# Optimization experiments

Hardware: AMD Instinct MI355X
Metric: run time of the kernel (lower is better)

## Reference

```python
import jax, jax.numpy as jnp
import numpy as np

B, NQ, L, E, K = 64, 1024, 128, 8192, 2
LN_EPS = 1e-5


def setup_inputs() -> dict:
    key = jax.random.key(0)
    ks = jax.random.split(key, 16)
    s1 = 1.0 / np.sqrt(2 * L + 1)
    s2 = 1.0 / np.sqrt(L)
    s3 = 1.0 / np.sqrt(2 * L)
    return {
        "z0": jax.random.normal(ks[0], (B, L), jnp.float32),
        "edge_index": jax.random.randint(ks[1], (2, E), 0, NQ, jnp.int64),
        "edge_attr": jax.random.normal(ks[2], (E,), jnp.float32),
        "n_qubits": NQ,
        # edge MLP params, stacked over K message-passing rounds
        "e_w1": jax.random.normal(ks[3], (K, L, 2 * L + 1), jnp.float32) * s1,
        "e_b1": jnp.zeros((K, L), jnp.float32),
        "e_w2": jax.random.normal(ks[4], (K, L, L), jnp.float32) * s2,
        "e_b2": jnp.zeros((K, L), jnp.float32),
        # node MLP params
        "n_w1": jax.random.normal(ks[5], (K, L, 2 * L), jnp.float32) * s3,
        "n_b1": jnp.zeros((K, L), jnp.float32),
        "ln_g": jnp.ones((K, L), jnp.float32),
        "ln_b": jnp.zeros((K, L), jnp.float32),
        "n_w2": jax.random.normal(ks[6], (K, L, L), jnp.float32) * s2,
        "n_b2": jnp.zeros((K, L), jnp.float32),
    }


def reference(z0, edge_index, edge_attr, n_qubits,
              e_w1, e_b1, e_w2, e_b2,
              n_w1, n_b1, ln_g, ln_b, n_w2, n_b2):
    b, l = z0.shape
    src, tgt = edge_index[0], edge_index[1]
    e_ = src.shape[0]
    # broadcast latent z0 to every node: h [B, N, L]
    h = jnp.broadcast_to(z0[:, None, :], (b, n_qubits, l))
    e = jnp.broadcast_to(edge_attr[None, :, None], (b, e_, 1))  # [B, E, 1]
    k_rounds = e_w1.shape[0]
    for k in range(k_rounds):
        hi = h[:, src, :]  # gather source node feats [B, E, L]
        hj = h[:, tgt, :]  # gather target node feats [B, E, L]
        inp_e = jnp.concatenate([hi, hj, e], axis=-1)  # [B, E, 2L+1]
        m = jax.nn.relu(inp_e @ e_w1[k].T + e_b1[k]) @ e_w2[k].T + e_b2[k]
        # scatter_add messages back to source nodes
        m_agg = jnp.zeros_like(h).at[:, src, :].add(m)
        inp_n = jnp.concatenate([h, m_agg], axis=-1)  # [B, N, 2L]
        x = jax.nn.relu(inp_n @ n_w1[k].T + n_b1[k])
        mu = x.mean(axis=-1, keepdims=True)
        var = ((x - mu) ** 2).mean(axis=-1, keepdims=True)
        x = (x - mu) * jax.lax.rsqrt(var + LN_EPS) * ln_g[k] + ln_b[k]
        # Dropout(p=0.1) is identity in eval mode
        h = x @ n_w2[k].T + n_b2[k] + h  # residual
    return h.mean(axis=1)  # [B, L]
```

## Files before the change

### kernel.cpp

```cpp
#include <hip/hip_runtime.h>

#define B_   64
#define NQ_  1024
#define L_   128
#define E_   8192
#define M_   (B_*NQ_)
#define LDP  136
#define TILE 2176

typedef unsigned short u16;
typedef unsigned int   u32;
typedef __attribute__((ext_vector_type(8))) short short8;
typedef __attribute__((ext_vector_type(4))) float floatx4;

#define WVB() __builtin_amdgcn_wave_barrier()

__device__ __forceinline__ u16 f2bf(float f) {
    union { float f; u32 u; } v; v.f = f;
    return (u16)((v.u + 0x7fffu + ((v.u >> 16) & 1u)) >> 16);
}
__device__ __forceinline__ float bf2f(u16 u) {
    union { u32 u; float f; } v; v.u = ((u32)u) << 16;
    return v.f;
}
__device__ __forceinline__ floatx4 mfma16(short8 a, short8 b, floatx4 c) {
    return __builtin_amdgcn_mfma_f32_16x16x32_bf16(a, b, c, 0, 0, 0);
}
__device__ __forceinline__ short8 gfrag(const u16* base, int r0, int kb, int lane) {
    return *(const short8*)(base + (size_t)(r0 + (lane & 15)) * 128 + kb * 32 + (lane >> 4) * 8);
}
__device__ __forceinline__ short8 sfrag(const u16* t, int r0, int kb, int lane) {
    return *(const short8*)(t + (r0 + (lane & 15)) * LDP + kb * 32 + (lane >> 4) * 8);
}
__device__ __forceinline__ short8 wfrag(const u16* wf, int nt, int kb, int lane) {
    return *(const short8*)(wf + (((kb << 3) + nt) * 64 + lane) * 8);
}
__device__ __forceinline__ void frag_flush(const u16* t, u16* wf, int nt, int lane) {
#pragma unroll
    for (int kb = 0; kb < 4; ++kb)
        *(short8*)(wf + (((kb << 3) + nt) * 64 + lane) * 8) = sfrag(t, 0, kb, lane);
}
__device__ __forceinline__ short8 frag_cvt(const float* base, int r0, int ld, int kb, int lane) {
    const float* p = base + (size_t)(r0 + (lane & 15)) * ld + kb * 32 + (lane >> 4) * 8;
    short8 s;
#pragma unroll
    for (int j = 0; j < 8; ++j) s[j] = (short)f2bf(p[j]);
    return s;
}
__device__ __forceinline__ void tile_store(u16* t, const floatx4* acc, int lane) {
    int col = lane & 15, qd = lane >> 4;
#pragma unroll
    for (int nt = 0; nt < 8; ++nt)
#pragma unroll
        for (int r = 0; r < 4; ++r)
            t[(qd * 4 + r) * LDP + nt * 16 + col] = f2bf(acc[nt][r]);
}
__device__ __forceinline__ void tile_flush(const u16* t, u16* g, int lane) {
#pragma unroll
    for (int it = 0; it < 4; ++it) {
        int chunk = it * 64 + lane, row = chunk >> 4, c8 = chunk & 15;
        *(uint4*)(g + (size_t)row * 128 + c8 * 8) = *(const uint4*)(t + row * LDP + c8 * 8);
    }
}

struct P {
    const int* ei; const float* attr; const float* z0;
    const float* e_w1; const float* e_b1; const float* e_w2; const float* e_b2;
    const float* n_w1; const float* n_b1; const float* ln_g; const float* ln_b;
    const float* n_w2; const float* n_b2;
    int* ofs; int* tgt_s; float* a_s; float* degf;
    u16* wf;
    u16* w_n20;
    float* wl; float* vb2;
    float* rx; float* rci; float* rcj; float* rh; float* mx0;
    u16* c0t; u16* S; u16* t1g; u16* ci1; u16* cj1;
    float* out;
};

__global__ __launch_bounds__(256) void k_setup(P p) {
    __shared__ __align__(16) char smem[52224];
    int tid = threadIdx.x, blk = blockIdx.x;
    int lane = tid & 63, w = tid >> 6, col = lane & 15, qd = lane >> 4;

    if (blk == 0) {
        int* cnt  = (int*)smem;
        int* wsum = cnt + 1024;
        int* flag = wsum + 8;
#pragma unroll
        for (int i = 0; i < 4; ++i) cnt[tid + i * 256] = 0;
        if (tid == 0) *flag = 1;
        __syncthreads();
        if (tid < 100 && p.ei[2 * tid + 1] != 0) atomicAnd(flag, 0);
        __syncthreads();
        int i64 = *flag;
        for (int e = tid; e < E_; e += 256) {
            int s = i64 ? p.ei[2 * e] : p.ei[e];
            atomicAdd(&cnt[s], 1);
        }
        __syncthreads();
        int q0 = tid * 4;
        int c0 = cnt[q0], c1 = cnt[q0 + 1], c2 = cnt[q0 + 2], c3 = cnt[q0 + 3];
        int tsum = c0 + c1 + c2 + c3, incl = tsum;
#pragma unroll
        for (int o = 1; o < 64; o <<= 1) {
            int t = __shfl_up(incl, o, 64);
            if (lane >= o) incl += t;
        }
        if (lane == 63) wsum[w] = incl;
        __syncthreads();
        int wo = 0;
        for (int i = 0; i < w; ++i) wo += wsum[i];
        int base = wo + incl - tsum;
        p.ofs[q0] = base; p.ofs[q0 + 1] = base + c0;
        p.ofs[q0 + 2] = base + c0 + c1; p.ofs[q0 + 3] = base + c0 + c1 + c2;
        p.degf[q0] = (float)c0; p.degf[q0 + 1] = (float)c1;
        p.degf[q0 + 2] = (float)c2; p.degf[q0 + 3] = (float)c3;
        if (tid == 0) p.ofs[NQ_] = E_;
        __syncthreads();
        cnt[q0] = base; cnt[q0 + 1] = base + c0;
        cnt[q0 + 2] = base + c0 + c1; cnt[q0 + 3] = base + c0 + c1 + c2;
        __syncthreads();
        for (int e = tid; e < E_; e += 256) {
            int s = i64 ? p.ei[2 * e]        : p.ei[e];
            int t = i64 ? p.ei[2 * (E_ + e)] : p.ei[E_ + e];
            int pos = atomicAdd(&cnt[s], 1);
            p.tgt_s[pos] = t;
            p.a_s[pos]   = p.attr[e];
        }
    } else if (blk == 1) {
        for (int idx = tid; idx < 16384; idx += 256) p.w_n20[idx] = f2bf(p.n_w2[idx]);
    } else if (blk == 2) {
        const float* src = p.n_w2 + 16384;
        u16* dst = p.wf + 5 * 16384;
        for (int pr = w; pr < 32; pr += 4) {
            int kb = pr >> 3, nt = pr & 7;
            const float* s = src + (nt * 16 + (lane & 15)) * 128 + kb * 32 + (lane >> 4) * 8;
            short8 v;
#pragma unroll
            for (int j = 0; j < 8; ++j) v[j] = (short)f2bf(s[j]);
            *(short8*)(dst + (pr * 64 + lane) * 8) = v;
        }
    } else if (blk <= 7) {
        const float* Pm; const float* Q; int ldp; u16* D;
        switch (blk) {
            case 3: Pm = p.n_w1 + 128;             ldp = 256; Q = p.e_w2;         D = p.wf;             break;
            case 4: Pm = p.n_w1 + 32768 + 128;     ldp = 256; Q = p.e_w2 + 16384; D = p.wf + 4 * 16384; break;
            case 5: Pm = p.e_w1 + 128 * 257;       ldp = 257; Q = p.n_w2;         D = p.wf + 1 * 16384; break;
            case 6: Pm = p.e_w1 + 128 * 257 + 128; ldp = 257; Q = p.n_w2;         D = p.wf + 2 * 16384; break;
            default:Pm = p.n_w1 + 32768;           ldp = 256; Q = p.n_w2;         D = p.wf + 3 * 16384; break;
        }
        u16* qt = (u16*)smem;
        u16* tl = (u16*)(smem + 34816);
        for (int idx = tid; idx < 16384; idx += 256) {
            int c = idx >> 7, kd = idx & 127;
            qt[kd * LDP + c] = f2bf(Q[idx]);
        }
        __syncthreads();
        for (int t = 0; t < 2; ++t) {
            int r0 = (w * 2 + t) * 16;
            floatx4 acc[8] = {};
#pragma unroll
            for (int kb = 0; kb < 4; ++kb) {
                short8 a = frag_cvt(Pm, r0, ldp, kb, lane);
#pragma unroll
                for (int nt = 0; nt < 8; ++nt)
                    acc[nt] = mfma16(a, sfrag(qt, nt * 16, kb, lane), acc[nt]);
            }
            u16* slot = tl + w * TILE;
            tile_store(slot, acc, lane); WVB();
            frag_flush(slot, D, w * 2 + t, lane); WVB();
        }
    } else if (blk == 8) {
        int r0 = w * 16;
        floatx4 acc[8] = {};
#pragma unroll
        for (int kb = 0; kb < 4; ++kb) {
            short8 a = frag_cvt(p.z0, r0, 128, kb, lane);
#pragma unroll
            for (int nt = 0; nt < 8; ++nt)
                acc[nt] = mfma16(a, frag_cvt(p.n_w1, nt * 16, 256, kb, lane), acc[nt]);
        }
#pragma unroll
        for (int nt = 0; nt < 8; ++nt) {
            int cg = nt * 16 + col; float bv = p.n_b1[cg];
#pragma unroll
            for (int r = 0; r < 4; ++r) p.rx[(r0 + qd * 4 + r) * 128 + cg] = acc[nt][r] + bv;
        }
    } else if (blk <= 11) {
        int r0 = w * 16;
        const float* Wp; int ld; const float* bias; float* dst;
        if (blk == 9)       { Wp = p.e_w1 + 128 * 257;       ld = 257; bias = p.e_b1 + 128; dst = p.rci; }
        else if (blk == 10) { Wp = p.e_w1 + 128 * 257 + 128; ld = 257; bias = nullptr;      dst = p.rcj; }
        else                { Wp = p.n_w1 + 32768;           ld = 256; bias = p.n_b1 + 128; dst = p.rh;  }
        floatx4 acc[8] = {};
#pragma unroll
        for (int kb = 0; kb < 4; ++kb) {
            short8 a;
            int rr = (r0 + (lane & 15)) * 128, kk = kb * 32 + (lane >> 4) * 8;
#pragma unroll
            for (int j = 0; j < 8; ++j) a[j] = (short)f2bf(p.z0[rr + kk + j] + p.n_b2[kk + j]);
#pragma unroll
            for (int nt = 0; nt < 8; ++nt)
                acc[nt] = mfma16(a, frag_cvt(Wp, nt * 16, ld, kb, lane), acc[nt]);
        }
#pragma unroll
        for (int nt = 0; nt < 8; ++nt) {
            int cg = nt * 16 + col;
            float bv = bias ? bias[cg] : 0.0f;
#pragma unroll
            for (int r = 0; r < 4; ++r) dst[(r0 + qd * 4 + r) * 128 + cg] = acc[nt][r] + bv;
        }
    } else if (blk == 12) {
        u16* tl = (u16*)(smem + 34816);
        int r0 = w * 16;
        floatx4 a1[8] = {};
#pragma unroll
        for (int kb = 0; kb < 4; ++kb) {
            short8 a = frag_cvt(p.z0, r0, 128, kb, lane);
#pragma unroll
            for (int nt = 0; nt < 8; ++nt) {
                a1[nt] = mfma16(a, frag_cvt(p.e_w1,       nt * 16, 257, kb, lane), a1[nt]);
                a1[nt] = mfma16(a, frag_cvt(p.e_w1 + 128, nt * 16, 257, kb, lane), a1[nt]);
            }
        }
#pragma unroll
        for (int nt = 0; nt < 8; ++nt) {
            float bv = p.e_b1[nt * 16 + col];
#pragma unroll
            for (int r = 0; r < 4; ++r) a1[nt][r] += bv;
        }
        u16* slot = tl + w * TILE;
        tile_store(slot, a1, lane); WVB();
        tile_flush(slot, p.c0t + (size_t)r0 * 128, lane);
    } else if (blk == 13) {
        int k = tid >> 7, c = tid & 127;
        float s = 0.0f;
        for (int n = 0; n < 128; ++n)
            s += p.n_w1[k * 32768 + c * 256 + 128 + n] * p.e_b2[k * 128 + n];
        p.vb2[tid] = s;
        p.wl[tid]  = p.e_w1[k * 128 * 257 + c * 257 + 256];
        for (int i = tid; i < 8192; i += 256) p.mx0[i] = 0.0f;
    }
}

__global__ __launch_bounds__(256) void k_edge(P p, int r0) {
    int tid = threadIdx.x, lane = tid & 63, w = tid >> 6;
    const u16* ci = r0 ? p.c0t : p.ci1;
    const u16* cj = p.cj1;
    const float* wl = r0 ? p.wl : p.wl + 128;
    float2 wl2 = ((const float2*)wl)[lane];
    int gw = blockIdx.x * 4 + w;
    int q = gw & (NQ_ - 1), bg = gw >> 10;
    int bl[8];
#pragma unroll
    for (int i = 0; i < 4; ++i) { bl[i] = bg * 4 + i; bl[i + 4] = bg * 4 + i + 32; }
    int st = p.ofs[q], en = p.ofs[q + 1];
    float ax[8] = {}, ay[8] = {};
    if (r0) {
        float cx[8], cy[8];
#pragma unroll
        for (int i = 0; i < 8; ++i) {
            u32 cv = ((const u32*)ci)[(size_t)bl[i] * 64 + lane];
            cx[i] = bf2f((u16)(cv & 0xffff)); cy[i] = bf2f((u16)(cv >> 16));
        }
        for (int idx = st; idx < en; ++idx) {
            float a = p.a_s[idx];
            float wx = a * wl2.x, wy = a * wl2.y;
#pragma unroll
            for (int i = 0; i < 8; ++i) {
                ax[i] += fmaxf(cx[i] + wx, 0.f);
                ay[i] += fmaxf(cy[i] + wy, 0.f);
            }
        }
    } else {
        const u32* cjp[8];
        float cx[8], cy[8];
#pragma unroll
        for (int i = 0; i < 8; ++i) {
            cjp[i] = (const u32*)cj + (size_t)bl[i] * NQ_ * 64;
            u32 cv = ((const u32*)ci)[((size_t)bl[i] * NQ_ + q) * 64 + lane];
            cx[i] = bf2f((u16)(cv & 0xffff)); cy[i] = bf2f((u16)(cv >> 16));
        }
        for (int idx = st; idx < en; ++idx) {
            int t = p.tgt_s[idx];
            float a = p.a_s[idx];
            size_t ro = (size_t)t * 64 + lane;
            float wx = a * wl2.x, wy = a * wl2.y;
#pragma unroll
            for (int i = 0; i < 8; ++i) {
                u32 jv = cjp[i][ro];
                ax[i] += fmaxf(cx[i] + bf2f((u16)(jv & 0xffff)) + wx, 0.f);
                ay[i] += fmaxf(cy[i] + bf2f((u16)(jv >> 16))    + wy, 0.f);
            }
        }
    }
    u32* Sp = (u32*)p.S;
#pragma unroll
    for (int i = 0; i < 8; ++i)
        Sp[((size_t)bl[i] * NQ_ + q) * 64 + lane] =
            (u32)f2bf(ax[i]) | ((u32)f2bf(ay[i]) << 16);
}

__global__ __launch_bounds__(256, 2) void k_node0(P p) {
    __shared__ __align__(16) char smem[52224];
    u16* xt = (u16*)smem;
    u16* ob = (u16*)(smem + 34816);
    int tid = threadIdx.x, lane = tid & 63, w = tid >> 6;
    int col = lane & 15, qd = lane >> 4;
    int blk = blockIdx.x;
    int rowbase = blk * 128 + w * 32;
    int b = blk >> 3;

    floatx4 xa[2][8] = {};
#pragma unroll
    for (int kb = 0; kb < 4; ++kb) {
        short8 Bv[8];
#pragma unroll
        for (int nt = 0; nt < 8; ++nt) Bv[nt] = wfrag(p.wf, nt, kb, lane);
#pragma unroll
        for (int t = 0; t < 2; ++t) {
            short8 a = gfrag(p.S, rowbase + t * 16, kb, lane);
#pragma unroll
            for (int nt = 0; nt < 8; ++nt) xa[t][nt] = mfma16(a, Bv[nt], xa[t][nt]);
        }
    }
    float s8[8] = {};
#pragma unroll
    for (int t = 0; t < 2; ++t) {
#pragma unroll
        for (int nt = 0; nt < 8; ++nt) {
            int cg = nt * 16 + col;
            float base = p.rx[b * 128 + cg], vb = p.vb2[cg];
#pragma unroll
            for (int r = 0; r < 4; ++r) {
                int row = rowbase + t * 16 + qd * 4 + r;
                xa[t][nt][r] = fmaxf(xa[t][nt][r] + base + p.degf[row & (NQ_ - 1)] * vb, 0.f);
            }
        }
#pragma unroll
        for (int r = 0; r < 4; ++r) {
            float s = 0.f, s2 = 0.f;
#pragma unroll
            for (int nt = 0; nt < 8; ++nt) { float v = xa[t][nt][r]; s += v; s2 += v * v; }
#pragma unroll
            for (int o = 1; o < 16; o <<= 1) { s += __shfl_xor(s, o, 64); s2 += __shfl_xor(s2, o, 64); }
            float mu = s * (1.f / 128.f), var = s2 * (1.f / 128.f) - mu * mu;
            float rs = rsqrtf(var + 1e-5f);
#pragma unroll
            for (int nt = 0; nt < 8; ++nt) {
                int cg = nt * 16 + col;
                float xv = (xa[t][nt][r] - mu) * rs * p.ln_g[cg] + p.ln_b[cg];
                xa[t][nt][r] = xv;
                s8[nt] += xv;
            }
        }
        tile_store(xt + (w * 2 + t) * TILE, xa[t], lane);
    }
#pragma unroll
    for (int nt = 0; nt < 8; ++nt) {
        s8[nt] += __shfl_xor(s8[nt], 16, 64);
        s8[nt] += __shfl_xor(s8[nt], 32, 64);
    }
    if (lane < 16) {
#pragma unroll
        for (int nt = 0; nt < 8; ++nt)
            atomicAdd(p.mx0 + b * 128 + nt * 16 + lane, s8[nt]);
    }
    WVB();
#pragma unroll
    for (int ph = 0; ph < 3; ++ph) {
        const u16* wfp = p.wf + ((ph == 0) ? 1 : (ph == 1) ? 2 : 3) * 16384;
        const float* rt = (ph == 0) ? p.rci : (ph == 1) ? p.rcj : p.rh;
        floatx4 ca[2][8] = {};
#pragma unroll
        for (int kb = 0; kb < 4; ++kb) {
            short8 Bv[8];
#pragma unroll
            for (int nt = 0; nt < 8; ++nt) Bv[nt] = wfrag(wfp, nt, kb, lane);
#pragma unroll
            for (int t = 0; t < 2; ++t) {
                short8 a = sfrag(xt + (w * 2 + t) * TILE, 0, kb, lane);
#pragma unroll
                for (int nt = 0; nt < 8; ++nt) ca[t][nt] = mfma16(a, Bv[nt], ca[t][nt]);
            }
        }
#pragma unroll
        for (int t = 0; t < 2; ++t)
#pragma unroll
            for (int nt = 0; nt < 8; ++nt) {
                float rc = rt[b * 128 + nt * 16 + col];
#pragma unroll
                for (int r = 0; r < 4; ++r) ca[t][nt][r] += rc;
            }
        u16* dst = (ph == 0) ? p.ci1 : (ph == 1) ? p.cj1 : p.t1g;
#pragma unroll
        for (int t = 0; t < 2; ++t) {
            tile_store(ob + w * TILE, ca[t], lane);
            WVB();
            tile_flush(ob + w * TILE, dst + (size_t)(rowbase + t * 16) * 128, lane);
            WVB();
        }
    }
}

__global__ __launch_bounds__(256, 2) void k_node1(P p) {
    __shared__ __align__(16) char smem[52224];
    u16* ob = (u16*)(smem + 34816);
    int tid = threadIdx.x, lane = tid & 63, w = tid >> 6;
    int col = lane & 15, qd = lane >> 4;
    int blk = blockIdx.x;
    int rowbase = blk * 128 + w * 32;
    int b = blk >> 3;

    const u16* wc1 = p.wf + 4 * 16384;
    floatx4 xa[2][8] = {};
#pragma unroll
    for (int kb = 0; kb < 4; ++kb) {
        short8 Bv[8];
#pragma unroll
        for (int nt = 0; nt < 8; ++nt) Bv[nt] = wfrag(wc1, nt, kb, lane);
#pragma unroll
        for (int t = 0; t < 2; ++t) {
            short8 a = gfrag(p.S, rowbase + t * 16, kb, lane);
#pragma unroll
            for (int nt = 0; nt < 8; ++nt) xa[t][nt] = mfma16(a, Bv[nt], xa[t][nt]);
        }
    }
    const float* vb21 = p.vb2 + 128;
#pragma unroll
    for (int t = 0; t < 2; ++t) {
#pragma unroll
        for (int nt = 0; nt < 8; ++nt) {
            int cg = nt * 16 + col;
            float vb = vb21[cg];
#pragma unroll
            for (int r = 0; r < 4; ++r) {
                int row = rowbase + t * 16 + qd * 4 + r;
                float tv = bf2f(p.t1g[(size_t)row * 128 + cg]);
                xa[t][nt][r] = fmaxf(xa[t][nt][r] + tv + p.degf[row & (NQ_ - 1)] * vb, 0.f);
            }
        }
#pragma unroll
        for (int r = 0; r < 4; ++r) {
            float s = 0.f, s2 = 0.f;
#pragma unroll
            for (int nt = 0; nt < 8; ++nt) { float v = xa[t][nt][r]; s += v; s2 += v * v; }
#pragma unroll
            for (int o = 1; o < 16; o <<= 1) { s += __shfl_xor(s, o, 64); s2 += __shfl_xor(s2, o, 64); }
            float mu = s * (1.f / 128.f), var = s2 * (1.f / 128.f) - mu * mu;
            float rs = rsqrtf(var + 1e-5f);
#pragma unroll
            for (int nt = 0; nt < 8; ++nt) {
                int cg = nt * 16 + col;
                xa[t][nt][r] = (xa[t][nt][r] - mu) * rs * p.ln_g[128 + cg] + p.ln_b[128 + cg];
            }
        }
    }
    const u16* n21 = p.wf + 5 * 16384;
    float s8[8] = {};
#pragma unroll
    for (int t = 0; t < 2; ++t) {
        WVB();
        tile_store(ob + w * TILE, xa[t], lane);
        WVB();
        floatx4 ma[8] = {};
#pragma unroll
        for (int kb = 0; kb < 4; ++kb) {
            short8 Bv[8];
#pragma unroll
            for (int nt = 0; nt < 8; ++nt) Bv[nt] = wfrag(n21, nt, kb, lane);
            short8 a = sfrag(ob + w * TILE, 0, kb, lane);
#pragma unroll
            for (int nt = 0; nt < 8; ++nt) ma[nt] = mfma16(a, Bv[nt], ma[nt]);
        }
#pragma unroll
        for (int nt = 0; nt < 8; ++nt)
#pragma unroll
            for (int r = 0; r < 4; ++r) s8[nt] += ma[nt][r];
    }
#pragma unroll
    for (int nt = 0; nt < 8; ++nt) {
        s8[nt] += __shfl_xor(s8[nt], 16, 64);
        s8[nt] += __shfl_xor(s8[nt], 32, 64);
    }
    if (lane < 16) {
#pragma unroll
        for (int nt = 0; nt < 8; ++nt)
            atomicAdd(p.out + b * 128 + nt * 16 + lane, s8[nt] * (1.f / 1024.f));
    }
    if ((blk & 7) == 0 && tid < 128) {
        int c = tid;
        const float* mx = p.mx0 + b * 128;
        float s = 0.f;
#pragma unroll 4
        for (int k = 0; k < 128; ++k) s += mx[k] * bf2f(p.w_n20[c * 128 + k]);
        float acc = p.z0[b * 128 + c] + p.n_b2[c] + p.n_b2[128 + c] + s * (1.f / 1024.f);
        atomicAdd(p.out + b * 128 + c, acc);
    }
}

extern "C" void kernel_launch(void* const* d_in, const int* in_sizes, int n_in,
                              void* d_out, int out_size, void* d_ws, size_t ws_size,
                              hipStream_t stream) {
    P p;
    p.z0   = (const float*)d_in[0];
    p.ei   = (const int*)d_in[1];
    p.attr = (const float*)d_in[2];
    p.e_w1 = (const float*)d_in[4];
    p.e_b1 = (const float*)d_in[5];
    p.e_w2 = (const float*)d_in[6];
    p.e_b2 = (const float*)d_in[7];
    p.n_w1 = (const float*)d_in[8];
    p.n_b1 = (const float*)d_in[9];
    p.ln_g = (const float*)d_in[10];
    p.ln_b = (const float*)d_in[11];
    p.n_w2 = (const float*)d_in[12];
    p.n_b2 = (const float*)d_in[13];
    p.out  = (float*)d_out;

    const size_t H = (size_t)M_ * L_;
    float* f  = (float*)d_ws;
    p.degf = f;
    p.a_s  = f + 1024;
    p.wl   = p.a_s + 8192;
    p.vb2  = p.wl + 256;
    p.rx   = p.vb2 + 256;
    p.rci  = p.rx + 8192;
    p.rcj  = p.rci + 8192;
    p.rh   = p.rcj + 8192;
    p.mx0  = p.rh + 8192;
    p.ofs  = (int*)(p.mx0 + 8192);
    p.tgt_s = p.ofs + 1056;
    p.wf    = (u16*)(p.tgt_s + 8192);
    p.w_n20 = p.wf + 6 * 16384;
    p.c0t   = p.w_n20 + 16384;
    p.S     = p.c0t + 8192;
    p.t1g   = p.S + H;
    p.ci1   = p.t1g + H;
    p.cj1   = p.ci1 + H;

    hipMemsetAsync(p.out, 0, 8192 * sizeof(float), stream);

    k_setup<<<14, 256, 0, stream>>>(p);
    k_edge<<<2048, 256, 0, stream>>>(p, 1);
    k_node0<<<512, 256, 0, stream>>>(p);
    k_edge<<<2048, 256, 0, stream>>>(p, 0);
    k_node1<<<512, 256, 0, stream>>>(p);
}
```

Baseline: 192.4 us.

## Fuse round-0 edge aggregation into node0 kernel, computing A fragments in registers

The round-0 edge message sum depends only on the per-batch latent and the edge attribute, so node0 now computes the aggregated S values directly into MFMA A-fragments in registers. This replaces a separate k_edge launch and the write and read of the S buffer through global memory. The edge kernel is specialised to the round-1 path only. In exchange each lane recomputes per-edge ReLU sums for its rows, which adds ALU work and register pressure inside node0.

```diff
diff --git a/kernel.cpp b/kernel.cpp
--- a/kernel.cpp
+++ b/kernel.cpp
@@ -243,11 +243,9 @@
     }
 }
 
-__global__ __launch_bounds__(256) void k_edge(P p, int r0) {
+__global__ __launch_bounds__(256) void k_edge(P p) {
     int tid = threadIdx.x, lane = tid & 63, w = tid >> 6;
-    const u16* ci = r0 ? p.c0t : p.ci1;
-    const u16* cj = p.cj1;
-    const float* wl = r0 ? p.wl : p.wl + 128;
+    const float* wl = p.wl + 128;
     float2 wl2 = ((const float2*)wl)[lane];
     int gw = blockIdx.x * 4 + w;
     int q = gw & (NQ_ - 1), bg = gw >> 10;
@@ -256,42 +254,24 @@
     for (int i = 0; i < 4; ++i) { bl[i] = bg * 4 + i; bl[i + 4] = bg * 4 + i + 32; }
     int st = p.ofs[q], en = p.ofs[q + 1];
     float ax[8] = {}, ay[8] = {};
-    if (r0) {
-        float cx[8], cy[8];
+    const u32* cjp[8];
+    float cx[8], cy[8];
+#pragma unroll
+    for (int i = 0; i < 8; ++i) {
+        cjp[i] = (const u32*)p.cj1 + (size_t)bl[i] * NQ_ * 64;
+        u32 cv = ((const u32*)p.ci1)[((size_t)bl[i] * NQ_ + q) * 64 + lane];
+        cx[i] = bf2f((u16)(cv & 0xffff)); cy[i] = bf2f((u16)(cv >> 16));
+    }
+    for (int idx = st; idx < en; ++idx) {
+        int t = p.tgt_s[idx];
+        float a = p.a_s[idx];
+        size_t ro = (size_t)t * 64 + lane;
+        float wx = a * wl2.x, wy = a * wl2.y;
 #pragma unroll
         for (int i = 0; i < 8; ++i) {
-            u32 cv = ((const u32*)ci)[(size_t)bl[i] * 64 + lane];
-            cx[i] = bf2f((u16)(cv & 0xffff)); cy[i] = bf2f((u16)(cv >> 16));
-        }
-        for (int idx = st; idx < en; ++idx) {
-            float a = p.a_s[idx];
-            float wx = a * wl2.x, wy = a * wl2.y;
-#pragma unroll
-            for (int i = 0; i < 8; ++i) {
-                ax[i] += fmaxf(cx[i] + wx, 0.f);
-                ay[i] += fmaxf(cy[i] + wy, 0.f);
-            }
-        }
-    } else {
-        const u32* cjp[8];
-        float cx[8], cy[8];
-#pragma unroll
-        for (int i = 0; i < 8; ++i) {
-            cjp[i] = (const u32*)cj + (size_t)bl[i] * NQ_ * 64;
-            u32 cv = ((const u32*)ci)[((size_t)bl[i] * NQ_ + q) * 64 + lane];
-            cx[i] = bf2f((u16)(cv & 0xffff)); cy[i] = bf2f((u16)(cv >> 16));
-        }
-        for (int idx = st; idx < en; ++idx) {
-            int t = p.tgt_s[idx];
-            float a = p.a_s[idx];
-            size_t ro = (size_t)t * 64 + lane;
-            float wx = a * wl2.x, wy = a * wl2.y;
-#pragma unroll
-            for (int i = 0; i < 8; ++i) {
-                u32 jv = cjp[i][ro];
-                ax[i] += fmaxf(cx[i] + bf2f((u16)(jv & 0xffff)) + wx, 0.f);
-                ay[i] += fmaxf(cy[i] + bf2f((u16)(jv >> 16))    + wy, 0.f);
-            }
+            u32 jv = cjp[i][ro];
+            ax[i] += fmaxf(cx[i] + bf2f((u16)(jv & 0xffff)) + wx, 0.f);
+            ay[i] += fmaxf(cy[i] + bf2f((u16)(jv >> 16))    + wy, 0.f);
         }
     }
     u32* Sp = (u32*)p.S;
@@ -311,6 +291,39 @@
     int rowbase = blk * 128 + w * 32;
     int b = blk >> 3;
 
+    short8 af[2][4];
+    {
+        float wlf[4][8], c0f[4][8];
+#pragma unroll
+        for (int kb = 0; kb < 4; ++kb) {
+            const float* wp = p.wl + kb * 32 + qd * 8;
+            const u16*  cp = p.c0t + b * 128 + kb * 32 + qd * 8;
+#pragma unroll
+            for (int j = 0; j < 8; ++j) { wlf[kb][j] = wp[j]; c0f[kb][j] = bf2f(cp[j]); }
+        }
+#pragma unroll
+        for (int t = 0; t < 2; ++t) {
+            int q = (rowbase + t * 16 + col) & (NQ_ - 1);
+            int st = p.ofs[q], en = p.ofs[q + 1];
+            float Sv[4][8] = {};
+            for (int idx = st; idx < en; ++idx) {
+                float a = p.a_s[idx];
+#pragma unroll
+                for (int kb = 0; kb < 4; ++kb)
+#pragma unroll
+                    for (int j = 0; j < 8; ++j)
+                        Sv[kb][j] += fmaxf(fmaf(a, wlf[kb][j], c0f[kb][j]), 0.f);
+            }
+#pragma unroll
+            for (int kb = 0; kb < 4; ++kb) {
+                short8 v;
+#pragma unroll
+                for (int j = 0; j < 8; ++j) v[j] = (short)f2bf(Sv[kb][j]);
+                af[t][kb] = v;
+            }
+        }
+    }
+
     floatx4 xa[2][8] = {};
 #pragma unroll
     for (int kb = 0; kb < 4; ++kb) {
@@ -318,11 +331,9 @@
 #pragma unroll
         for (int nt = 0; nt < 8; ++nt) Bv[nt] = wfrag(p.wf, nt, kb, lane);
 #pragma unroll
-        for (int t = 0; t < 2; ++t) {
-            short8 a = gfrag(p.S, rowbase + t * 16, kb, lane);
-#pragma unroll
-            for (int nt = 0; nt < 8; ++nt) xa[t][nt] = mfma16(a, Bv[nt], xa[t][nt]);
-        }
+        for (int t = 0; t < 2; ++t)
+#pragma unroll
+            for (int nt = 0; nt < 8; ++nt) xa[t][nt] = mfma16(af[t][kb], Bv[nt], xa[t][nt]);
     }
     float s8[8] = {};
 #pragma unroll
@@ -542,8 +553,7 @@
     hipMemsetAsync(p.out, 0, 8192 * sizeof(float), stream);
 
     k_setup<<<14, 256, 0, stream>>>(p);
-    k_edge<<<2048, 256, 0, stream>>>(p, 1);
     k_node0<<<512, 256, 0, stream>>>(p);
-    k_edge<<<2048, 256, 0, stream>>>(p, 0);
+    k_edge<<<2048, 256, 0, stream>>>(p);
     k_node1<<<512, 256, 0, stream>>>(p);
 }
```

Result: no change. 191.7 us (-0.4%).
